# Performance work log

Hardware: AMD Instinct MI355X
Metric: run time of the kernel (lower is better)

## Reference

```python
import jax, jax.numpy as jnp
import numpy as np

CONF_THRES = 0.4
IOU_THRES = 0.45
MAX_WH = 4096.0   # class offset for non-agnostic NMS (torch code: max_wh)
K_PRE = 1024      # candidates kept for the O(K^2) NMS stage (<= max_nms=30000)
MAX_DET = 300     # max detections per image (torch default)
B, N, NC = 16, 25200, 80


def xywh2xyxy(x):
    xy, wh = x[..., :2], x[..., 2:4]
    return jnp.concatenate([xy - wh * 0.5, xy + wh * 0.5], axis=-1)


def box_iou(a, b):
    # a: [K,4], b: [K,4] in xyxy
    area_a = (a[:, 2] - a[:, 0]) * (a[:, 3] - a[:, 1])
    area_b = (b[:, 2] - b[:, 0]) * (b[:, 3] - b[:, 1])
    lt = jnp.maximum(a[:, None, :2], b[None, :, :2])
    rb = jnp.minimum(a[:, None, 2:], b[None, :, 2:])
    inter = jnp.clip(rb - lt, 0.0, None).prod(-1)
    return inter / (area_a[:, None] + area_b[None, :] - inter + 1e-7)


def _nms_single(pred, conf_logit, logit, head):
    # pred [N,85] (decoded, sigmoided), conf_logit [N,5] raw, logit [N,80] raw, head [N]
    xc = pred[:, 4] > CONF_THRES                      # objectness gate
    obj_sig = jax.nn.sigmoid(conf_logit[:, 4:5])      # [N,1]
    log_sig = jax.nn.sigmoid(logit) * obj_sig         # sel_prob == 'objclass'
    cls_scores = pred[:, 5:] * pred[:, 4:5]           # x[:,5:] *= x[:,4:5]
    box = xywh2xyxy(pred[:, :4])                      # [N,4]
    conf = cls_scores.max(axis=1)                     # best class conf
    j = cls_scores.argmax(axis=1).astype(pred.dtype)  # best class id
    valid = xc & (conf > CONF_THRES)
    score = jnp.where(valid, conf, 0.0)
    # top-K candidates (sorted descending) -> fixed-shape NMS
    top_s, top_i = jax.lax.top_k(score, K_PRE)
    valid_k = top_s > 0.0
    boxes_k = box[top_i] + j[top_i, None] * MAX_WH    # per-class box offset (agnostic=False)
    iou = box_iou(boxes_k, boxes_k)                   # [K,K]
    idx = jnp.arange(K_PRE)

    def body(i, keep):
        sup = (iou[i] > IOU_THRES) & (idx > i) & keep[i]
        return keep & ~sup

    keep = jax.lax.fori_loop(0, K_PRE, body, valid_k)
    final_score = jnp.where(keep, top_s, 0.0)
    _, sel = jax.lax.top_k(final_score, MAX_DET)      # first MAX_DET survivors
    gi = top_i[sel]
    m = (final_score[sel] > 0.0).astype(pred.dtype)[:, None]  # validity mask
    det = jnp.concatenate([box[gi], conf[gi, None], j[gi, None]], axis=1)  # [300,6] xyxy,conf,cls
    # pack: det(6) | class logits*obj(80) | obj_conf(1) | classHead(1) | valid(1) -> [300,89]
    return jnp.concatenate(
        [det * m, log_sig[gi] * m, obj_sig[gi] * m, head[gi, None] * m, m], axis=1)


def setup_inputs() -> dict:
    key = jax.random.key(0)
    k1, k2, k3, k4, k5, k6 = jax.random.split(key, 6)
    xy = jax.random.uniform(k1, (B, N, 2), jnp.float32) * 640.0
    wh = 2.0 + jax.random.uniform(k2, (B, N, 2), jnp.float32) * 198.0
    objcls = jax.random.uniform(k3, (B, N, 1 + NC), jnp.float32)
    prediction = jnp.concatenate([xy, wh, objcls], axis=-1)       # [B,N,85]
    pred_conf_logits = jax.random.normal(k4, (B, N, 5), jnp.float32)
    logits = jax.random.normal(k5, (B, N, NC), jnp.float32)
    class_head = jax.random.randint(k6, (B, N), 0, 3).astype(jnp.float32)
    return {"prediction": prediction, "pred_conf_logits": pred_conf_logits,
            "logits": logits, "class_head": class_head}


def reference(prediction, pred_conf_logits, logits, class_head):
    return jax.vmap(_nms_single)(prediction, pred_conf_logits, logits, class_head)
```

## Files before the change

### kernel.cpp

```cpp
#include <hip/hip_runtime.h>
#include <math.h>

#define BATCH 16
#define NN 25200
#define NCLS 80
#define K_PRE 1024
#define MAX_DET 300
#define CONF_T 0.4f
#define IOU_T 0.45f
#define TBIAS 0x3E000000u
#define RROWS 128
#define OUT_STRIDE 26700
#define SCR_KEYS_OFF 0
#define SCR_S_OFF    16384
#define SCR_BC_OFF   20480

__global__ void __launch_bounds__(512) score_kernel(
    const float* __restrict__ pred, unsigned long long* __restrict__ keys,
    unsigned* __restrict__ ghist, float* __restrict__ out) {
    const int tid = threadIdx.x;
    const int r = tid >> 2, sub = tid & 3;
    const int n = blockIdx.x * RROWS + r;
    const int b = blockIdx.y;

    if (blockIdx.x == 196) {
        unsigned* bc = (unsigned*)((char*)(out + (size_t)b * OUT_STRIDE) +
                                   SCR_BC_OFF);
        bc[tid] = 0u;
        bc[tid + 512] = 0u;
    }

    float best = 0.0f;
    int bc_i = sub * 20;
    float obj = 0.0f;
    if (n < NN) {
        const float* row = pred + ((size_t)b * NN + n) * 85;
        obj = row[4];
        if (obj > CONF_T) {
            const float* cp = row + 5 + sub * 20;
#pragma unroll
            for (int i = 0; i < 5; ++i) {
                float4 v4 = *reinterpret_cast<const float4*>(cp + 4 * i);
                float v;
                v = v4.x * obj;
                if (v > best) { best = v; bc_i = sub * 20 + 4 * i + 0; }
                v = v4.y * obj;
                if (v > best) { best = v; bc_i = sub * 20 + 4 * i + 1; }
                v = v4.z * obj;
                if (v > best) { best = v; bc_i = sub * 20 + 4 * i + 2; }
                v = v4.w * obj;
                if (v > best) { best = v; bc_i = sub * 20 + 4 * i + 3; }
            }
        }
    }
#pragma unroll
    for (int d = 1; d < 4; d <<= 1) {
        float ov = __shfl_xor(best, d);
        int oc = __shfl_xor(bc_i, d);
        if (ov > best || (ov == best && oc < bc_i)) { best = ov; bc_i = oc; }
    }
    if (n < NN && sub == 0) {
        unsigned t = (obj > CONF_T && best > CONF_T)
                         ? (__float_as_uint(best) - TBIAS) : 0u;
        keys[(size_t)b * NN + n] =
            ((unsigned long long)t << 22) |
            ((unsigned long long)(unsigned)(NN - 1 - n) << 7) |
            (unsigned)bc_i;
        if (t) atomicAdd(&ghist[b * 1024 + (t >> 15)], 1u);
    }
}

__global__ void __launch_bounds__(1024) select_kernel(
    const unsigned long long* __restrict__ keys,
    const unsigned* __restrict__ ghist, float* __restrict__ out) {
    __shared__ unsigned sA[1024], sB[1024];
    const int c = blockIdx.x, b = blockIdx.y, tid = threadIdx.x;
    char* scratch = (char*)(out + (size_t)b * OUT_STRIDE);
    unsigned long long* gsk = (unsigned long long*)(scratch + SCR_KEYS_OFF);
    unsigned* gS = (unsigned*)(scratch + SCR_S_OFF);
    unsigned* gBC = (unsigned*)(scratch + SCR_BC_OFF);

    sA[tid] = ghist[b * 1024 + tid];
    __syncthreads();
    unsigned* src = sA;
    unsigned* dst = sB;
    for (int off = 1; off < 1024; off <<= 1) {
        dst[tid] = src[tid] + ((tid + off < 1024) ? src[tid + off] : 0u);
        __syncthreads();
        unsigned* t2 = src; src = dst; dst = t2;
    }
    if (c == 0) gS[tid] = src[tid];

    int i = c * 1024 + tid;
    if (i < NN) {
        unsigned long long key = keys[(size_t)b * NN + i];
        unsigned t = (unsigned)(key >> 22);
        if (t) {
            unsigned d = t >> 15;
            unsigned base = (d < 1023u) ? src[d + 1] : 0u;
            if (base < 1024u) {
                unsigned pos = base + atomicAdd(&gBC[d], 1u);
                if (pos < 2048u) gsk[pos] = key;
            }
        }
    }
}

__global__ void __launch_bounds__(1024) nms_out_kernel(
    const float* __restrict__ pred, const float* __restrict__ conf_logits,
    const float* __restrict__ logits, const float* __restrict__ head,
    float* __restrict__ out) {
    __shared__ unsigned sS[1024];
    __shared__ unsigned sA[1024], sB[1024];
    __shared__ unsigned long long skeys[2048];
    __shared__ float bx0[K_PRE], by0[K_PRE], bx1[K_PRE], by1[K_PRE],
        bar_[K_PRE], bsc[K_PRE];
    __shared__ unsigned char bcls[K_PRE];
    __shared__ unsigned short bgi[K_PRE];
    __shared__ unsigned char bkeep[K_PRE];
    __shared__ unsigned sel_dmin;

    const int b = blockIdx.x, tid = threadIdx.x;
    char* scratch = (char*)(out + (size_t)b * OUT_STRIDE);
    const unsigned long long* gsk =
        (const unsigned long long*)(scratch + SCR_KEYS_OFF);
    const unsigned* gS = (const unsigned*)(scratch + SCR_S_OFF);

    sS[tid] = gS[tid];
    if (tid == 0) sel_dmin = 0u;
    __syncthreads();
    {
        unsigned base_d = (tid < 1023) ? sS[tid + 1] : 0u;
        if (base_d < 1024u && (tid == 0 || sS[tid] >= 1024u))
            sel_dmin = (unsigned)tid;
    }
    __syncthreads();
    const unsigned M = sS[sel_dmin];
    const unsigned Mc = M < 2048u ? M : 2048u;

#pragma unroll
    for (int half = 0; half < 2; ++half) {
        int i = tid + (half << 10);
        skeys[i] = ((unsigned)i < Mc) ? gsk[i] : 0ull;
    }
    bcls[tid] = 255;
    bsc[tid] = 0.0f;
    bkeep[tid] = 0;
    __syncthreads();

#pragma unroll
    for (int half = 0; half < 2; ++half) {
        int i = tid + (half << 10);
        unsigned long long key = skeys[i];
        if (key) {
            unsigned t = (unsigned)(key >> 22);
            unsigned d = t >> 15;
            unsigned seg = (d < 1023u) ? sS[d + 1] : 0u;
            unsigned end = sS[d];
            if (end > 2048u) end = 2048u;
            unsigned r = seg;
            for (unsigned j = seg; j < end; ++j)
                if (skeys[j] > key) ++r;
            if (r < 1024u) {
                int n = NN - 1 - (int)((key >> 7) & 32767u);
                const float* row = pred + ((size_t)b * NN + n) * 85;
                float x = row[0], y = row[1], w = row[2], h = row[3];
                float vx0 = x - w * 0.5f, vy0 = y - h * 0.5f;
                float vx1 = x + w * 0.5f, vy1 = y + h * 0.5f;
                bx0[r] = vx0; by0[r] = vy0; bx1[r] = vx1; by1[r] = vy1;
                bar_[r] = (vx1 - vx0) * (vy1 - vy0);
                bsc[r] = __uint_as_float(t + TBIAS);
                bcls[r] = (unsigned char)(key & 127u);
                bgi[r] = (unsigned short)n;
            }
        }
    }
    __syncthreads();

    {
        const int lane = tid & 63;
        const int wv = tid >> 6;
        unsigned char myc[16];
#pragma unroll
        for (int k = 0; k < 16; ++k) myc[k] = bcls[(k << 6) | lane];

        for (int ci = 0; ci < 5; ++ci) {
            const int c = wv + (ci << 4);
            unsigned alive = 0u;
#pragma unroll
            for (int k = 0; k < 16; ++k)
                if (myc[k] == (unsigned char)c) alive |= (1u << k);
            unsigned keptm = 0u;
            for (;;) {
                int s = alive ? ((__builtin_ctz(alive) << 6) | lane)
                              : (1 << 30);
#pragma unroll
                for (int d = 32; d; d >>= 1) {
                    int o = __shfl_xor(s, d);
                    s = o < s ? o : s;
                }
                if (s >= (1 << 30)) break;
                if ((s & 63) == lane) {
                    alive &= ~(1u << (s >> 6));
                    keptm |= (1u << (s >> 6));
                }
                float ax0 = bx0[s], ay0 = by0[s], ax1 = bx1[s], ay1 = by1[s];
                float aa = bar_[s];
                unsigned rem = alive;
                while (rem) {
                    int k = __builtin_ctz(rem);
                    rem &= rem - 1;
                    int j = (k << 6) | lane;
                    float lx = fmaxf(ax0, bx0[j]);
                    float ly = fmaxf(ay0, by0[j]);
                    float rx = fminf(ax1, bx1[j]);
                    float ry = fminf(ay1, by1[j]);
                    float iw = fmaxf(rx - lx, 0.0f);
                    float ih = fmaxf(ry - ly, 0.0f);
                    float inter = iw * ih;
                    float iou = inter / (aa + bar_[j] - inter + 1e-7f);
                    if (iou > IOU_T) alive &= ~(1u << k);
                }
            }
            while (keptm) {
                int k = __builtin_ctz(keptm);
                keptm &= keptm - 1;
                bkeep[(k << 6) | lane] = 1;
            }
        }
    }
    __syncthreads();

    int kp = (int)bkeep[tid];
    unsigned* src = sA;
    unsigned* dst = sB;
    src[tid] = (unsigned)kp;
    __syncthreads();
    for (int off = 1; off < 1024; off <<= 1) {
        dst[tid] = src[tid] + ((tid >= off) ? src[tid - off] : 0u);
        __syncthreads();
        unsigned* t2 = src; src = dst; dst = t2;
    }
    int rank = (int)src[tid] - kp;
    int kcnt = (int)src[1023];

    if (kp && rank < MAX_DET) {
        int gi = (int)bgi[tid];
        float* orow = out + ((size_t)b * MAX_DET + rank) * 89;
        orow[0] = bx0[tid]; orow[1] = by0[tid];
        orow[2] = bx1[tid]; orow[3] = by1[tid];
        orow[4] = bsc[tid];
        orow[5] = (float)bcls[tid];
        float cl = conf_logits[((size_t)b * NN + gi) * 5 + 4];
        float obj_sig = 1.0f / (1.0f + expf(-cl));
        const float4* lrow4 =
            (const float4*)(logits + ((size_t)b * NN + gi) * NCLS);
#pragma unroll 4
        for (int q = 0; q < 20; ++q) {
            float4 l4 = lrow4[q];
            orow[6 + 4 * q + 0] = obj_sig / (1.0f + expf(-l4.x));
            orow[6 + 4 * q + 1] = obj_sig / (1.0f + expf(-l4.y));
            orow[6 + 4 * q + 2] = obj_sig / (1.0f + expf(-l4.z));
            orow[6 + 4 * q + 3] = obj_sig / (1.0f + expf(-l4.w));
        }
        orow[86] = obj_sig;
        orow[87] = head[(size_t)b * NN + gi];
        orow[88] = 1.0f;
    }
    if (tid < MAX_DET && tid >= kcnt) {
        float* orow = out + ((size_t)b * MAX_DET + tid) * 89;
#pragma unroll
        for (int q = 0; q < 89; ++q) orow[q] = 0.0f;
    }
}

extern "C" void kernel_launch(void* const* d_in, const int* in_sizes, int n_in,
                              void* d_out, int out_size, void* d_ws,
                              size_t ws_size, hipStream_t stream) {
    const float* pred        = (const float*)d_in[0];
    const float* conf_logits = (const float*)d_in[1];
    const float* logits      = (const float*)d_in[2];
    const float* head        = (const float*)d_in[3];
    float* out = (float*)d_out;

    char* ws = (char*)d_ws;
    unsigned long long* keys = (unsigned long long*)ws;
    unsigned* ghist = (unsigned*)(ws + (size_t)BATCH * NN * 8);

    hipMemsetAsync(ghist, 0, (size_t)BATCH * 1024 * sizeof(unsigned), stream);

    dim3 sgrid((NN + RROWS - 1) / RROWS, BATCH);
    score_kernel<<<sgrid, 512, 0, stream>>>(pred, keys, ghist, out);
    dim3 cgrid(25, BATCH);
    select_kernel<<<cgrid, 1024, 0, stream>>>(keys, ghist, out);
    nms_out_kernel<<<BATCH, 1024, 0, stream>>>(pred, conf_logits, logits,
                                               head, out);
}
```

Measured before the change: 355.3 us.

## Split candidate ranking into a separate kernel and use ballot-based NMS pivot selection

The rank-and-gather of the top candidates moves out of the single-block-per-image NMS kernel into a new prep_kernel with 2 blocks per image, which writes boxes, areas, scores, classes and indices to scratch. The candidate count M is now computed once in select_kernel. In the NMS loop, boxes are laid out so each lane owns 16 contiguous entries, which lets the pivot be picked with one ballot and one shuffle instead of a six-step shuffle-min reduction. The cost is an extra kernel launch, plus rank counting that now reads keys from global memory instead of LDS.

```diff
diff --git a/kernel.cpp b/kernel.cpp
--- a/kernel.cpp
+++ b/kernel.cpp
@@ -14,6 +14,15 @@
 #define SCR_KEYS_OFF 0
 #define SCR_S_OFF    16384
 #define SCR_BC_OFF   20480
+#define SCR_M_OFF    24576
+#define SCR_X0_OFF   28672
+#define SCR_Y0_OFF   32768
+#define SCR_X1_OFF   36864
+#define SCR_Y1_OFF   40960
+#define SCR_AR_OFF   45056
+#define SCR_SC_OFF   49152
+#define SCR_CL_OFF   53248
+#define SCR_GI_OFF   57344
 
 __global__ void __launch_bounds__(512) score_kernel(
     const float* __restrict__ pred, unsigned long long* __restrict__ keys,
@@ -74,12 +83,14 @@
     const unsigned long long* __restrict__ keys,
     const unsigned* __restrict__ ghist, float* __restrict__ out) {
     __shared__ unsigned sA[1024], sB[1024];
+    __shared__ unsigned sel_dmin;
     const int c = blockIdx.x, b = blockIdx.y, tid = threadIdx.x;
     char* scratch = (char*)(out + (size_t)b * OUT_STRIDE);
     unsigned long long* gsk = (unsigned long long*)(scratch + SCR_KEYS_OFF);
     unsigned* gS = (unsigned*)(scratch + SCR_S_OFF);
     unsigned* gBC = (unsigned*)(scratch + SCR_BC_OFF);
 
+    if (tid == 0) sel_dmin = 0u;
     sA[tid] = ghist[b * 1024 + tid];
     __syncthreads();
     unsigned* src = sA;
@@ -89,7 +100,15 @@
         __syncthreads();
         unsigned* t2 = src; src = dst; dst = t2;
     }
-    if (c == 0) gS[tid] = src[tid];
+    if (c == 0) {
+        gS[tid] = src[tid];
+        unsigned base_d = (tid < 1023) ? src[tid + 1] : 0u;
+        if (base_d < 1024u && (tid == 0 || src[tid] >= 1024u))
+            sel_dmin = (unsigned)tid;
+        __syncthreads();
+        if (tid == 0)
+            *(unsigned*)(scratch + SCR_M_OFF) = src[sel_dmin];
+    }
 
     int i = c * 1024 + tid;
     if (i < NN) {
@@ -106,75 +125,72 @@
     }
 }
 
-__global__ void __launch_bounds__(1024) nms_out_kernel(
-    const float* __restrict__ pred, const float* __restrict__ conf_logits,
-    const float* __restrict__ logits, const float* __restrict__ head,
-    float* __restrict__ out) {
-    __shared__ unsigned sS[1024];
-    __shared__ unsigned sA[1024], sB[1024];
-    __shared__ unsigned long long skeys[2048];
-    __shared__ float bx0[K_PRE], by0[K_PRE], bx1[K_PRE], by1[K_PRE],
-        bar_[K_PRE], bsc[K_PRE];
-    __shared__ unsigned char bcls[K_PRE];
-    __shared__ unsigned short bgi[K_PRE];
-    __shared__ unsigned char bkeep[K_PRE];
-    __shared__ unsigned sel_dmin;
-
-    const int b = blockIdx.x, tid = threadIdx.x;
+__global__ void __launch_bounds__(1024) prep_kernel(
+    const float* __restrict__ pred, float* __restrict__ out) {
+    const int b = blockIdx.y;
+    const int i = blockIdx.x * 1024 + threadIdx.x;
     char* scratch = (char*)(out + (size_t)b * OUT_STRIDE);
     const unsigned long long* gsk =
         (const unsigned long long*)(scratch + SCR_KEYS_OFF);
     const unsigned* gS = (const unsigned*)(scratch + SCR_S_OFF);
-
-    sS[tid] = gS[tid];
-    if (tid == 0) sel_dmin = 0u;
-    __syncthreads();
-    {
-        unsigned base_d = (tid < 1023) ? sS[tid + 1] : 0u;
-        if (base_d < 1024u && (tid == 0 || sS[tid] >= 1024u))
-            sel_dmin = (unsigned)tid;
-    }
-    __syncthreads();
-    const unsigned M = sS[sel_dmin];
+    const unsigned M = *(const unsigned*)(scratch + SCR_M_OFF);
     const unsigned Mc = M < 2048u ? M : 2048u;
 
-#pragma unroll
-    for (int half = 0; half < 2; ++half) {
-        int i = tid + (half << 10);
-        skeys[i] = ((unsigned)i < Mc) ? gsk[i] : 0ull;
-    }
-    bcls[tid] = 255;
-    bsc[tid] = 0.0f;
+    if ((unsigned)i >= Mc) {
+        if (i < 1024) {
+            ((int*)(scratch + SCR_CL_OFF))[i] = 255;
+            ((float*)(scratch + SCR_SC_OFF))[i] = 0.0f;
+        }
+        return;
+    }
+    unsigned long long key = gsk[i];
+    unsigned t = (unsigned)(key >> 22);
+    unsigned d = t >> 15;
+    unsigned seg = (d < 1023u) ? gS[d + 1] : 0u;
+    unsigned end = gS[d];
+    if (end > 2048u) end = 2048u;
+    unsigned r = seg;
+    for (unsigned j = seg; j < end; ++j)
+        if (gsk[j] > key) ++r;
+    if (r < 1024u) {
+        int n = NN - 1 - (int)((key >> 7) & 32767u);
+        const float* row = pred + ((size_t)b * NN + n) * 85;
+        float x = row[0], y = row[1], w = row[2], h = row[3];
+        float vx0 = x - w * 0.5f, vy0 = y - h * 0.5f;
+        float vx1 = x + w * 0.5f, vy1 = y + h * 0.5f;
+        ((float*)(scratch + SCR_X0_OFF))[r] = vx0;
+        ((float*)(scratch + SCR_Y0_OFF))[r] = vy0;
+        ((float*)(scratch + SCR_X1_OFF))[r] = vx1;
+        ((float*)(scratch + SCR_Y1_OFF))[r] = vy1;
+        ((float*)(scratch + SCR_AR_OFF))[r] = (vx1 - vx0) * (vy1 - vy0);
+        ((float*)(scratch + SCR_SC_OFF))[r] = __uint_as_float(t + TBIAS);
+        ((int*)(scratch + SCR_CL_OFF))[r] = (int)(key & 127u);
+        ((int*)(scratch + SCR_GI_OFF))[r] = n;
+    }
+}
+
+__global__ void __launch_bounds__(1024) nms_out_kernel(
+    const float* __restrict__ conf_logits, const float* __restrict__ logits,
+    const float* __restrict__ head, float* __restrict__ out) {
+    __shared__ unsigned sA[1024], sB[1024];
+    __shared__ float bx0[K_PRE], by0[K_PRE], bx1[K_PRE], by1[K_PRE],
+        bar_[K_PRE];
+    __shared__ unsigned char bcls[K_PRE];
+    __shared__ unsigned char bkeep[K_PRE];
+
+    const int b = blockIdx.x, tid = threadIdx.x;
+    char* scratch = (char*)(out + (size_t)b * OUT_STRIDE);
+
+    bx0[tid] = ((const float*)(scratch + SCR_X0_OFF))[tid];
+    by0[tid] = ((const float*)(scratch + SCR_Y0_OFF))[tid];
+    bx1[tid] = ((const float*)(scratch + SCR_X1_OFF))[tid];
+    by1[tid] = ((const float*)(scratch + SCR_Y1_OFF))[tid];
+    bar_[tid] = ((const float*)(scratch + SCR_AR_OFF))[tid];
+    int mycls = ((const int*)(scratch + SCR_CL_OFF))[tid];
+    float mysc = ((const float*)(scratch + SCR_SC_OFF))[tid];
+    int mygi = ((const int*)(scratch + SCR_GI_OFF))[tid];
+    bcls[tid] = (unsigned char)mycls;
     bkeep[tid] = 0;
-    __syncthreads();
-
-#pragma unroll
-    for (int half = 0; half < 2; ++half) {
-        int i = tid + (half << 10);
-        unsigned long long key = skeys[i];
-        if (key) {
-            unsigned t = (unsigned)(key >> 22);
-            unsigned d = t >> 15;
-            unsigned seg = (d < 1023u) ? sS[d + 1] : 0u;
-            unsigned end = sS[d];
-            if (end > 2048u) end = 2048u;
-            unsigned r = seg;
-            for (unsigned j = seg; j < end; ++j)
-                if (skeys[j] > key) ++r;
-            if (r < 1024u) {
-                int n = NN - 1 - (int)((key >> 7) & 32767u);
-                const float* row = pred + ((size_t)b * NN + n) * 85;
-                float x = row[0], y = row[1], w = row[2], h = row[3];
-                float vx0 = x - w * 0.5f, vy0 = y - h * 0.5f;
-                float vx1 = x + w * 0.5f, vy1 = y + h * 0.5f;
-                bx0[r] = vx0; by0[r] = vy0; bx1[r] = vx1; by1[r] = vy1;
-                bar_[r] = (vx1 - vx0) * (vy1 - vy0);
-                bsc[r] = __uint_as_float(t + TBIAS);
-                bcls[r] = (unsigned char)(key & 127u);
-                bgi[r] = (unsigned short)n;
-            }
-        }
-    }
     __syncthreads();
 
     {
@@ -182,7 +198,7 @@
         const int wv = tid >> 6;
         unsigned char myc[16];
 #pragma unroll
-        for (int k = 0; k < 16; ++k) myc[k] = bcls[(k << 6) | lane];
+        for (int k = 0; k < 16; ++k) myc[k] = bcls[(lane << 4) | k];
 
         for (int ci = 0; ci < 5; ++ci) {
             const int c = wv + (ci << 4);
@@ -192,17 +208,15 @@
                 if (myc[k] == (unsigned char)c) alive |= (1u << k);
             unsigned keptm = 0u;
             for (;;) {
-                int s = alive ? ((__builtin_ctz(alive) << 6) | lane)
-                              : (1 << 30);
-#pragma unroll
-                for (int d = 32; d; d >>= 1) {
-                    int o = __shfl_xor(s, d);
-                    s = o < s ? o : s;
-                }
-                if (s >= (1 << 30)) break;
-                if ((s & 63) == lane) {
-                    alive &= ~(1u << (s >> 6));
-                    keptm |= (1u << (s >> 6));
+                unsigned long long bal = __ballot(alive != 0u);
+                if (!bal) break;
+                int ls = (int)__builtin_ctzll(bal);
+                int cand = alive ? ((lane << 4) | __builtin_ctz(alive)) : 0;
+                int s = __shfl(cand, ls);
+                if (lane == ls) {
+                    int kk = __builtin_ctz(alive);
+                    alive &= ~(1u << kk);
+                    keptm |= (1u << kk);
                 }
                 float ax0 = bx0[s], ay0 = by0[s], ax1 = bx1[s], ay1 = by1[s];
                 float aa = bar_[s];
@@ -210,7 +224,7 @@
                 while (rem) {
                     int k = __builtin_ctz(rem);
                     rem &= rem - 1;
-                    int j = (k << 6) | lane;
+                    int j = (lane << 4) | k;
                     float lx = fmaxf(ax0, bx0[j]);
                     float ly = fmaxf(ay0, by0[j]);
                     float rx = fminf(ax1, bx1[j]);
@@ -225,7 +239,7 @@
             while (keptm) {
                 int k = __builtin_ctz(keptm);
                 keptm &= keptm - 1;
-                bkeep[(k << 6) | lane] = 1;
+                bkeep[(lane << 4) | k] = 1;
             }
         }
     }
@@ -245,16 +259,15 @@
     int kcnt = (int)src[1023];
 
     if (kp && rank < MAX_DET) {
-        int gi = (int)bgi[tid];
         float* orow = out + ((size_t)b * MAX_DET + rank) * 89;
         orow[0] = bx0[tid]; orow[1] = by0[tid];
         orow[2] = bx1[tid]; orow[3] = by1[tid];
-        orow[4] = bsc[tid];
-        orow[5] = (float)bcls[tid];
-        float cl = conf_logits[((size_t)b * NN + gi) * 5 + 4];
+        orow[4] = mysc;
+        orow[5] = (float)mycls;
+        float cl = conf_logits[((size_t)b * NN + mygi) * 5 + 4];
         float obj_sig = 1.0f / (1.0f + expf(-cl));
         const float4* lrow4 =
-            (const float4*)(logits + ((size_t)b * NN + gi) * NCLS);
+            (const float4*)(logits + ((size_t)b * NN + mygi) * NCLS);
 #pragma unroll 4
         for (int q = 0; q < 20; ++q) {
             float4 l4 = lrow4[q];
@@ -264,7 +277,7 @@
             orow[6 + 4 * q + 3] = obj_sig / (1.0f + expf(-l4.w));
         }
         orow[86] = obj_sig;
-        orow[87] = head[(size_t)b * NN + gi];
+        orow[87] = head[(size_t)b * NN + mygi];
         orow[88] = 1.0f;
     }
     if (tid < MAX_DET && tid >= kcnt) {
@@ -293,6 +306,8 @@
     score_kernel<<<sgrid, 512, 0, stream>>>(pred, keys, ghist, out);
     dim3 cgrid(25, BATCH);
     select_kernel<<<cgrid, 1024, 0, stream>>>(keys, ghist, out);
-    nms_out_kernel<<<BATCH, 1024, 0, stream>>>(pred, conf_logits, logits,
-                                               head, out);
-}
+    dim3 pgrid(2, BATCH);
+    prep_kernel<<<pgrid, 1024, 0, stream>>>(pred, out);
+    nms_out_kernel<<<BATCH, 1024, 0, stream>>>(conf_logits, logits, head,
+                                               out);
+}
```

After: 354.7 us. No clear change (-0.2%).
